# Kernel optimization log

Hardware: AMD Instinct MI355X
Metric: run time of the kernel (lower is better)

The kernel has to match this reference:

```python
import jax, jax.numpy as jnp
import numpy as np

BANDWIDTH = 1.0


def setup_inputs() -> dict:
    key = jax.random.key(0)
    k1, k2 = jax.random.split(key)
    test_data = jax.random.normal(k1, (8192, 512), dtype=jnp.float32)
    train_data = jax.random.normal(k2, (16384, 512), dtype=jnp.float32)
    return {"test_data": test_data, "train_data": train_data}


def reference(test_data, train_data):
    # test_data: [N, D], train_data: [M, D]
    bw = jnp.asarray(BANDWIDTH, dtype=test_data.dtype)
    n_train, d = train_data.shape
    # (avoids materializing the [N, M, D] difference tensor)
    x2 = jnp.sum(test_data * test_data, axis=-1, keepdims=True)        # [N, 1]
    y2 = jnp.sum(train_data * train_data, axis=-1)[None, :]           # [1, M]
    xy = jnp.einsum('nd,md->nm', test_data, train_data)               # [N, M]
    sq_dist = jnp.maximum(x2 + y2 - 2.0 * xy, 0.0)                    # [N, M]
    log_exp = -0.5 * sq_dist / (bw * bw)
    # normalization constant z = 0.5*d*log(2*pi) + d*log(bw) + log(n)
    z = (0.5 * d * jnp.log(jnp.asarray(2.0 * np.pi, dtype=test_data.dtype))
         + d * jnp.log(bw)
         + jnp.log(jnp.asarray(float(n_train), dtype=test_data.dtype)))
    return jax.scipy.special.logsumexp(log_exp - z, axis=-1)          # [N]
```

## Files before the change

kernel.cpp:

```cpp
#include <hip/hip_runtime.h>
#include <hip/hip_fp8.h>

#define D 512
#define NTEST 8192
#define NTRAIN 16384
#define BN 128
#define BM 128
#define KB 128
#define NCHUNK 8
#define NPART (NCHUNK * 2)
#define CHUNK_M (NTRAIN / NCHUNK)
#define TILES (CHUNK_M / BM)
#define ZCONST 480.20058952863157f

typedef __attribute__((ext_vector_type(4))) int int4v;
typedef __attribute__((ext_vector_type(8))) int int8v;
typedef __attribute__((ext_vector_type(4))) float floatx4;

__device__ __forceinline__ void async_copy16(const void* g, void* l) {
  __builtin_amdgcn_global_load_lds(
      (const __attribute__((address_space(1))) unsigned int*)g,
      (__attribute__((address_space(3))) unsigned int*)l, 16, 0, 0);
}

__global__ __launch_bounds__(256) void prep_kernel(
    const float* __restrict__ test, const float* __restrict__ train,
    unsigned char* __restrict__ testq, unsigned char* __restrict__ trainq,
    float* __restrict__ x2, float* __restrict__ y2) {
  const int gw = (int)((blockIdx.x * blockDim.x + threadIdx.x) >> 6);
  const int lane = threadIdx.x & 63;
  const float* src;
  unsigned char* dst;
  float* sq;
  if (gw < NTEST) {
    src = test + (size_t)gw * D;
    dst = testq + (size_t)gw * D;
    sq = x2 + gw;
  } else {
    const int r = gw - NTEST;
    src = train + (size_t)r * D;
    dst = trainq + (size_t)r * D;
    sq = y2 + r;
  }
  const int kb = lane >> 4;
  const int q = (lane >> 2) & 3;
  const int h = (lane >> 1) & 1;
  const int hb = lane & 1;
  const int sbase = kb * 128 + q * 32 + h * 16 + hb * 8;
  const int dbase = kb * 128 + h * 64 + q * 16 + hb * 8;
  float4 v0 = *(const float4*)(src + sbase);
  float4 v1 = *(const float4*)(src + sbase + 4);
  float s = v0.x * v0.x + v0.y * v0.y + v0.z * v0.z + v0.w * v0.w +
            v1.x * v1.x + v1.y * v1.y + v1.z * v1.z + v1.w * v1.w;
  float f[8] = {v0.x, v0.y, v0.z, v0.w, v1.x, v1.y, v1.z, v1.w};
  unsigned long long p = 0;
#pragma unroll
  for (int i = 0; i < 8; ++i) {
    __hip_fp8_e4m3 qv(f[i]);
    p |= (unsigned long long)qv.__x << (8 * i);
  }
  *(unsigned long long*)(dst + dbase) = p;
#pragma unroll
  for (int off = 32; off >= 1; off >>= 1) s += __shfl_xor(s, off);
  if (lane == 0) *sq = s;
}

__global__ __launch_bounds__(256, 2) void fused_kernel(
    const unsigned char* __restrict__ A, const unsigned char* __restrict__ B,
    const float* __restrict__ y2, float* __restrict__ part_m,
    float* __restrict__ part_l) {
  __shared__ unsigned char sA[BN * KB];
  __shared__ unsigned char sB[BM * KB];
  const int tid = threadIdx.x;
  const int lane = tid & 63;
  const int w = tid >> 6;
  const int lm = lane & 15;
  const int lk = lane >> 4;
  const int rowbase = blockIdx.x * BN;
  const int chunk = blockIdx.y;
  const int wrow = (w >> 1) * 64;
  const int wcol = (w & 1) * 64;

  float run_m[16], run_l[16];
#pragma unroll
  for (int i = 0; i < 16; ++i) { run_m[i] = -1e30f; run_l[i] = 0.f; }

  for (int t = 0; t < TILES; ++t) {
    const int colbase = chunk * CHUNK_M + t * BM;
    float y2v[4];
#pragma unroll
    for (int ct = 0; ct < 4; ++ct)
      y2v[ct] = y2[colbase + wcol + ct * 16 + lm];

    floatx4 acc[4][4];
#pragma unroll
    for (int rt = 0; rt < 4; ++rt)
#pragma unroll
      for (int ct = 0; ct < 4; ++ct)
        acc[rt][ct] = floatx4{0.f, 0.f, 0.f, 0.f};

    for (int kb = 0; kb < D / KB; ++kb) {
      __syncthreads();
#pragma unroll
      for (int i = 0; i < 4; ++i) {
        const int o = tid * 16 + i * 4096;
        const int r = o >> 7;
        const int csw = (o >> 4) & 7;
        const int off = ((csw ^ (r & 7)) << 4);
        async_copy16(A + (size_t)(rowbase + r) * D + kb * 128 + off, sA + o);
        async_copy16(B + (size_t)(colbase + r) * D + kb * 128 + off, sB + o);
      }
      __syncthreads();
      int8v af[4], bfr[4];
#pragma unroll
      for (int rt = 0; rt < 4; ++rt) {
        const int row = wrow + rt * 16 + lm;
        int4v lo = *(const int4v*)&sA[row * KB + ((lk ^ (row & 7)) << 4)];
        int4v hi = *(const int4v*)&sA[row * KB + (((4 + lk) ^ (row & 7)) << 4)];
        af[rt] = __builtin_shufflevector(lo, hi, 0, 1, 2, 3, 4, 5, 6, 7);
      }
#pragma unroll
      for (int ct = 0; ct < 4; ++ct) {
        const int row = wcol + ct * 16 + lm;
        int4v lo = *(const int4v*)&sB[row * KB + ((lk ^ (row & 7)) << 4)];
        int4v hi = *(const int4v*)&sB[row * KB + (((4 + lk) ^ (row & 7)) << 4)];
        bfr[ct] = __builtin_shufflevector(lo, hi, 0, 1, 2, 3, 4, 5, 6, 7);
      }
#pragma unroll
      for (int rt = 0; rt < 4; ++rt)
#pragma unroll
        for (int ct = 0; ct < 4; ++ct)
          acc[rt][ct] = __builtin_amdgcn_mfma_scale_f32_16x16x128_f8f6f4(
              af[rt], bfr[ct], acc[rt][ct], 0, 0, 0, 127, 0, 127);
    }

#pragma unroll
    for (int rt = 0; rt < 4; ++rt) {
#pragma unroll
      for (int reg = 0; reg < 4; ++reg) {
        const int idx = rt * 4 + reg;
        const float v0 = fmaf(-0.5f, y2v[0], acc[rt][0][reg]);
        const float v1 = fmaf(-0.5f, y2v[1], acc[rt][1][reg]);
        const float v2 = fmaf(-0.5f, y2v[2], acc[rt][2][reg]);
        const float v3 = fmaf(-0.5f, y2v[3], acc[rt][3][reg]);
        const float tmax = fmaxf(fmaxf(v0, v1), fmaxf(v2, v3));
        const float nm = fmaxf(run_m[idx], tmax);
        const float alpha = __expf(run_m[idx] - nm);
        const float ps = __expf(v0 - nm) + __expf(v1 - nm) +
                         __expf(v2 - nm) + __expf(v3 - nm);
        run_l[idx] = fmaf(run_l[idx], alpha, ps);
        run_m[idx] = nm;
      }
    }
  }

  const int slot = chunk * 2 + (w & 1);
#pragma unroll
  for (int rt = 0; rt < 4; ++rt) {
#pragma unroll
    for (int reg = 0; reg < 4; ++reg) {
      const int idx = rt * 4 + reg;
      float m = run_m[idx], l = run_l[idx];
#pragma unroll
      for (int off = 1; off < 16; off <<= 1) {
        const float om = __shfl_xor(m, off);
        const float ol = __shfl_xor(l, off);
        const float nm2 = fmaxf(m, om);
        l = l * __expf(m - nm2) + ol * __expf(om - nm2);
        m = nm2;
      }
      if (lm == 0) {
        const int grow = rowbase + wrow + rt * 16 + lk * 4 + reg;
        part_m[slot * NTEST + grow] = m;
        part_l[slot * NTEST + grow] = l;
      }
    }
  }
}

__global__ __launch_bounds__(256) void combine_kernel(
    const float* __restrict__ part_m, const float* __restrict__ part_l,
    const float* __restrict__ x2, float* __restrict__ out) {
  const int n = blockIdx.x * blockDim.x + threadIdx.x;
  if (n >= NTEST) return;
  float m[NPART];
  float mx = -1e30f;
#pragma unroll
  for (int c = 0; c < NPART; ++c) {
    m[c] = part_m[c * NTEST + n];
    mx = fmaxf(mx, m[c]);
  }
  float s = 0.f;
#pragma unroll
  for (int c = 0; c < NPART; ++c)
    s += part_l[c * NTEST + n] * __expf(m[c] - mx);
  out[n] = fmaf(-0.5f, x2[n], mx + __logf(s) - ZCONST);
}

extern "C" void kernel_launch(void* const* d_in, const int* in_sizes, int n_in,
                              void* d_out, int out_size, void* d_ws, size_t ws_size,
                              hipStream_t stream) {
  const float* test = (const float*)d_in[0];
  const float* train = (const float*)d_in[1];
  float* out = (float*)d_out;
  char* ws = (char*)d_ws;

  unsigned char* testq = (unsigned char*)ws;
  unsigned char* trainq = (unsigned char*)(ws + (size_t)NTEST * D);
  float* x2 = (float*)(ws + (size_t)(NTEST + NTRAIN) * D);
  float* y2 = x2 + NTEST;
  float* part_m = y2 + NTRAIN;
  float* part_l = part_m + NPART * NTEST;

  prep_kernel<<<(NTEST + NTRAIN) / 4, 256, 0, stream>>>(
      test, train, testq, trainq, x2, y2);
  fused_kernel<<<dim3(NTEST / BN, NCHUNK), 256, 0, stream>>>(
      testq, trainq, y2, part_m, part_l);
  combine_kernel<<<NTEST / 256, 256, 0, stream>>>(part_m, part_l, x2, out);
}
```

Measured before the change: 162.4 us.

## Double-buffer LDS tiles to overlap async global loads with MFMA compute

Splits the shared A and B tiles into two buffers and runs a software pipeline. The next K-slice (and the first slice of the next column tile) is issued with global_load_lds while the current slice feeds the MFMAs. This replaces the previous pattern of load, barrier, compute with two barriers per K step. Swizzled global and LDS offsets are also precomputed once per thread instead of every iteration. The cost is twice the LDS per block, which may limit occupancy, plus an extra barrier after the softmax epilogue.

```diff
diff --git a/kernel.cpp b/kernel.cpp
--- a/kernel.cpp
+++ b/kernel.cpp
@@ -69,8 +69,10 @@
     const unsigned char* __restrict__ A, const unsigned char* __restrict__ B,
     const float* __restrict__ y2, float* __restrict__ part_m,
     float* __restrict__ part_l) {
-  __shared__ unsigned char sA[BN * KB];
-  __shared__ unsigned char sB[BM * KB];
+  __shared__ unsigned char sA0[BN * KB];
+  __shared__ unsigned char sA1[BN * KB];
+  __shared__ unsigned char sB0[BM * KB];
+  __shared__ unsigned char sB1[BM * KB];
   const int tid = threadIdx.x;
   const int lane = tid & 63;
   const int w = tid >> 6;
@@ -81,58 +83,93 @@
   const int wrow = (w >> 1) * 64;
   const int wcol = (w & 1) * 64;
 
+  size_t aS[4], bS[4];
+  int dO[4];
+#pragma unroll
+  for (int i = 0; i < 4; ++i) {
+    const int o = tid * 16 + i * 4096;
+    const int r = o >> 7;
+    const int csw = (o >> 4) & 7;
+    const int off = ((csw ^ (r & 7)) << 4);
+    dO[i] = o;
+    aS[i] = (size_t)(rowbase + r) * D + off;
+    bS[i] = (size_t)r * D + off;
+  }
+  int aOffLo[4], aOffHi[4], bOffLo[4], bOffHi[4];
+#pragma unroll
+  for (int i = 0; i < 4; ++i) {
+    const int arow = wrow + i * 16 + lm;
+    aOffLo[i] = arow * KB + ((lk ^ (arow & 7)) << 4);
+    aOffHi[i] = arow * KB + (((4 + lk) ^ (arow & 7)) << 4);
+    const int brow = wcol + i * 16 + lm;
+    bOffLo[i] = brow * KB + ((lk ^ (brow & 7)) << 4);
+    bOffHi[i] = brow * KB + (((4 + lk) ^ (brow & 7)) << 4);
+  }
+
+  auto stage = [&](unsigned char* sa, unsigned char* sb, size_t bcolD,
+                   int kb) {
+#pragma unroll
+    for (int i = 0; i < 4; ++i) {
+      async_copy16(A + aS[i] + kb * 128, sa + dO[i]);
+      async_copy16(B + bcolD + bS[i] + kb * 128, sb + dO[i]);
+    }
+  };
+
+  floatx4 acc[4][4];
+  auto compute = [&](const unsigned char* sa, const unsigned char* sb) {
+    int8v af[4], bf[4];
+#pragma unroll
+    for (int rt = 0; rt < 4; ++rt) {
+      int4v lo = *(const int4v*)&sa[aOffLo[rt]];
+      int4v hi = *(const int4v*)&sa[aOffHi[rt]];
+      af[rt] = __builtin_shufflevector(lo, hi, 0, 1, 2, 3, 4, 5, 6, 7);
+    }
+#pragma unroll
+    for (int ct = 0; ct < 4; ++ct) {
+      int4v lo = *(const int4v*)&sb[bOffLo[ct]];
+      int4v hi = *(const int4v*)&sb[bOffHi[ct]];
+      bf[ct] = __builtin_shufflevector(lo, hi, 0, 1, 2, 3, 4, 5, 6, 7);
+    }
+#pragma unroll
+    for (int rt = 0; rt < 4; ++rt)
+#pragma unroll
+      for (int ct = 0; ct < 4; ++ct)
+        acc[rt][ct] = __builtin_amdgcn_mfma_scale_f32_16x16x128_f8f6f4(
+            af[rt], bf[ct], acc[rt][ct], 0, 0, 0, 127, 0, 127);
+  };
+
   float run_m[16], run_l[16];
 #pragma unroll
   for (int i = 0; i < 16; ++i) { run_m[i] = -1e30f; run_l[i] = 0.f; }
+
+  stage(sA0, sB0, (size_t)(chunk * CHUNK_M) * D, 0);
+  __syncthreads();
 
   for (int t = 0; t < TILES; ++t) {
     const int colbase = chunk * CHUNK_M + t * BM;
+    const size_t bcolD = (size_t)colbase * D;
     float y2v[4];
 #pragma unroll
     for (int ct = 0; ct < 4; ++ct)
       y2v[ct] = y2[colbase + wcol + ct * 16 + lm];
 
-    floatx4 acc[4][4];
 #pragma unroll
     for (int rt = 0; rt < 4; ++rt)
 #pragma unroll
       for (int ct = 0; ct < 4; ++ct)
         acc[rt][ct] = floatx4{0.f, 0.f, 0.f, 0.f};
 
-    for (int kb = 0; kb < D / KB; ++kb) {
-      __syncthreads();
-#pragma unroll
-      for (int i = 0; i < 4; ++i) {
-        const int o = tid * 16 + i * 4096;
-        const int r = o >> 7;
-        const int csw = (o >> 4) & 7;
-        const int off = ((csw ^ (r & 7)) << 4);
-        async_copy16(A + (size_t)(rowbase + r) * D + kb * 128 + off, sA + o);
-        async_copy16(B + (size_t)(colbase + r) * D + kb * 128 + off, sB + o);
-      }
-      __syncthreads();
-      int8v af[4], bfr[4];
-#pragma unroll
-      for (int rt = 0; rt < 4; ++rt) {
-        const int row = wrow + rt * 16 + lm;
-        int4v lo = *(const int4v*)&sA[row * KB + ((lk ^ (row & 7)) << 4)];
-        int4v hi = *(const int4v*)&sA[row * KB + (((4 + lk) ^ (row & 7)) << 4)];
-        af[rt] = __builtin_shufflevector(lo, hi, 0, 1, 2, 3, 4, 5, 6, 7);
-      }
-#pragma unroll
-      for (int ct = 0; ct < 4; ++ct) {
-        const int row = wcol + ct * 16 + lm;
-        int4v lo = *(const int4v*)&sB[row * KB + ((lk ^ (row & 7)) << 4)];
-        int4v hi = *(const int4v*)&sB[row * KB + (((4 + lk) ^ (row & 7)) << 4)];
-        bfr[ct] = __builtin_shufflevector(lo, hi, 0, 1, 2, 3, 4, 5, 6, 7);
-      }
-#pragma unroll
-      for (int rt = 0; rt < 4; ++rt)
-#pragma unroll
-        for (int ct = 0; ct < 4; ++ct)
-          acc[rt][ct] = __builtin_amdgcn_mfma_scale_f32_16x16x128_f8f6f4(
-              af[rt], bfr[ct], acc[rt][ct], 0, 0, 0, 127, 0, 127);
-    }
+    stage(sA1, sB1, bcolD, 1);
+    compute(sA0, sB0);
+    __syncthreads();
+    stage(sA0, sB0, bcolD, 2);
+    compute(sA1, sB1);
+    __syncthreads();
+    stage(sA1, sB1, bcolD, 3);
+    compute(sA0, sB0);
+    __syncthreads();
+    if (t + 1 < TILES) stage(sA0, sB0, bcolD + (size_t)BM * D, 0);
+    compute(sA1, sB1);
 
 #pragma unroll
     for (int rt = 0; rt < 4; ++rt) {
@@ -152,6 +189,7 @@
         run_m[idx] = nm;
       }
     }
+    __syncthreads();
   }
 
   const int slot = chunk * 2 + (w & 1);
```

Result: no change. 162.4 us (+0.0%).
